# Kernel tuning notes

Hardware: AMD Instinct MI355X
Metric: run time of the kernel (lower is better)

## Reference

```python
import jax, jax.numpy as jnp
import numpy as np

DIM = 2048
N_HEADS = 16
N_KV_HEADS = 4
HEAD_DIM = DIM // N_HEADS  # 128
ROPE_BASE = 10000.0
QK_GAIN_INIT = 1.0
RMS_EPS = 1.1920928955078125e-07  # torch F.rms_norm default eps = finfo(fp32).eps


def _rms_norm(x):
    # normalize over last dim, no learned gain
    var = jnp.mean(jnp.square(x), axis=-1, keepdims=True)
    return x * jax.lax.rsqrt(var + RMS_EPS)


def _rope_cos_sin(seq_len, dtype):
    half = HEAD_DIM // 2
    inv_freq = 1.0 / (ROPE_BASE ** (jnp.arange(0, HEAD_DIM, 2, dtype=jnp.float32) / HEAD_DIM))
    t = jnp.arange(seq_len, dtype=jnp.float32)
    freqs = jnp.outer(t, inv_freq)  # [S, half]
    return jnp.cos(freqs).astype(dtype), jnp.sin(freqs).astype(dtype)


def _apply_rotary(x, cos, sin):
    # x: [B, H, S, D]; cos/sin: [S, D//2] broadcast over B,H
    half = x.shape[-1] // 2
    x1, x2 = x[..., :half], x[..., half:]
    return jnp.concatenate((x1 * cos + x2 * sin, x1 * (-sin) + x2 * cos), axis=-1)


def setup_inputs() -> dict:
    key = jax.random.key(0)
    ks = jax.random.split(key, 6)
    B, S = 2, 2048
    kv_dim = N_KV_HEADS * HEAD_DIM
    x = jax.random.normal(ks[0], (B, S, DIM), dtype=jnp.float32)
    Wq = jax.random.normal(ks[1], (DIM, DIM), dtype=jnp.float32) * (DIM ** -0.5)
    Wk = jax.random.normal(ks[2], (kv_dim, DIM), dtype=jnp.float32) * (DIM ** -0.5)
    Wv = jax.random.normal(ks[3], (kv_dim, DIM), dtype=jnp.float32) * (DIM ** -0.5)
    Wproj = jax.random.normal(ks[4], (DIM, DIM), dtype=jnp.float32) * (DIM ** -0.5)
    q_gain = jnp.full((N_HEADS,), QK_GAIN_INIT, dtype=jnp.float32)
    return {"x": x, "Wq": Wq, "Wk": Wk, "Wv": Wv, "Wproj": Wproj, "q_gain": q_gain}


def reference(x, Wq, Wk, Wv, Wproj, q_gain):
    B, S, D = x.shape
    G = N_HEADS // N_KV_HEADS  # GQA group size
    # QKV projections (CastedLinear, no bias)
    q = (x @ Wq.T).reshape(B, S, N_HEADS, HEAD_DIM).transpose(0, 2, 1, 3)      # [B,H,S,d]
    k = (x @ Wk.T).reshape(B, S, N_KV_HEADS, HEAD_DIM).transpose(0, 2, 1, 3)   # [B,Hkv,S,d]
    v = (x @ Wv.T).reshape(B, S, N_KV_HEADS, HEAD_DIM).transpose(0, 2, 1, 3)
    # QK RMS-norm
    q = _rms_norm(q)
    k = _rms_norm(k)
    # RoPE (scaling='none' -> attention_factor = 1.0)
    cos, sin = _rope_cos_sin(S, q.dtype)
    q = _apply_rotary(q, cos, sin)
    k = _apply_rotary(k, cos, sin)
    # per-head query gain * attention_factor (=1.0)
    q = q * q_gain.astype(q.dtype)[None, :, None, None]
    # causal GQA SDPA: group queries by kv head, no k/v materialized repeats
    qg = q.reshape(B, N_KV_HEADS, G, S, HEAD_DIM)
    scale = 1.0 / jnp.sqrt(jnp.asarray(HEAD_DIM, dtype=q.dtype))
    scores = jnp.einsum('bkgqd,bkld->bkgql', qg, k) * scale  # [B,Hkv,G,S,S]
    causal = jnp.tril(jnp.ones((S, S), dtype=bool))
    scores = jnp.where(causal, scores, jnp.asarray(-jnp.inf, dtype=scores.dtype))
    attn = jax.nn.softmax(scores, axis=-1)
    y = jnp.einsum('bkgql,bkld->bkgqd', attn, v)              # [B,Hkv,G,S,d]
    y = y.reshape(B, N_HEADS, S, HEAD_DIM).transpose(0, 2, 1, 3).reshape(B, S, D)
    return y @ Wproj.T
```

## Files before the change

### kernel.cpp

```cpp
#include <hip/hip_runtime.h>
#include <hip/hip_bf16.h>

#define DIM 2048
#define NH 16
#define NKV 4
#define HD 128
#define S_LEN 2048
#define BATCH 2
#define QKV_N 3072
#define NEGBIG -1.0e30f

typedef __attribute__((ext_vector_type(8))) short bf16x8;
typedef __attribute__((ext_vector_type(4))) float f32x4;
typedef unsigned short ushort_t;

#define GLOAD_LDS16(gp, lp)                                                       \
    __builtin_amdgcn_global_load_lds(                                             \
        (const __attribute__((address_space(1))) void*)(gp),                      \
        (__attribute__((address_space(3))) void*)(lp), 16, 0, 0)

static __device__ __forceinline__ ushort_t f2bf(float f) {
    union { float f; unsigned u; } v; v.f = f;
    unsigned r = v.u + 0x7fffu + ((v.u >> 16) & 1u);
    return (ushort_t)(r >> 16);
}
static __device__ __forceinline__ float bf2f(ushort_t u) {
    union { unsigned u; float f; } v; v.u = ((unsigned)u) << 16;
    return v.f;
}
static __device__ __forceinline__ unsigned pk2bf(float a, float b) {
    unsigned r;
    __asm__ volatile("v_cvt_pk_bf16_f32 %0, %1, %2" : "=v"(r) : "v"(a), "v"(b));
    return r;
}

__global__ __launch_bounds__(256) void cvt_in(const float* __restrict__ x,
                                              const float* __restrict__ Wq,
                                              const float* __restrict__ Wk,
                                              const float* __restrict__ Wv,
                                              const float* __restrict__ Wp,
                                              ushort_t* __restrict__ xb,
                                              ushort_t* __restrict__ Wqkvb,
                                              ushort_t* __restrict__ Wpb) {
    int i = (blockIdx.x * 256 + threadIdx.x) * 4;
    const float* src;
    ushort_t* dst;
    int soff, doff;
    if (i < 8388608) {
        src = x; dst = xb; soff = i; doff = i;
    } else if (i < 14680064) {
        int j = i - 8388608;
        dst = Wqkvb; doff = j;
        if (j < 4194304) { src = Wq; soff = j; }
        else if (j < 5242880) { src = Wk; soff = j - 4194304; }
        else { src = Wv; soff = j - 5242880; }
    } else {
        int j = i - 14680064;
        src = Wp; dst = Wpb; soff = j; doff = j;
    }
    float4 v = *(const float4*)&src[soff];
    uint2 o = {pk2bf(v.x, v.y), pk2bf(v.z, v.w)};
    *(uint2*)&dst[doff] = o;
}

static __device__ __forceinline__ void store_c(float* p, float v) { *p = v; }
static __device__ __forceinline__ void store_c(ushort_t* p, float v) { *p = f2bf(v); }

template <typename OutT>
__global__ __launch_bounds__(256) void gemm_bt(const ushort_t* __restrict__ A,
                                               const ushort_t* __restrict__ B,
                                               OutT* __restrict__ C,
                                               int M, int N, int K) {
    __shared__ __align__(16) ushort_t As[128 * 64];
    __shared__ __align__(16) ushort_t Bs[128 * 64];
    const int t = threadIdx.x;
    const int lane = t & 63;
    const int wave = t >> 6;
    const int m16 = lane & 15;
    const int quad = lane >> 4;
    const int wr = wave >> 1;
    const int wc = wave & 1;
    const int m0 = blockIdx.y * 128;
    const int n0 = blockIdx.x * 128;

    f32x4 acc[4][4];
#pragma unroll
    for (int i = 0; i < 4; i++)
#pragma unroll
        for (int j = 0; j < 4; j++) acc[i][j] = (f32x4){0.f, 0.f, 0.f, 0.f};

    const int rsub = lane >> 3;
    const int csw0 = lane & 7;

    for (int k0 = 0; k0 < K; k0 += 64) {
#pragma unroll
        for (int i = 0; i < 4; ++i) {
            const int rowb = wave * 32 + i * 8;
            const int row = rowb + rsub;
            const int gc = (csw0 ^ (row & 7)) * 8;
            GLOAD_LDS16(&A[(size_t)(m0 + row) * K + k0 + gc], &As[rowb * 64]);
            GLOAD_LDS16(&B[(size_t)(n0 + row) * K + k0 + gc], &Bs[rowb * 64]);
        }
        __syncthreads();
#pragma unroll
        for (int ks = 0; ks < 2; ks++) {
            bf16x8 af[4], bfr[4];
#pragma unroll
            for (int mt = 0; mt < 4; mt++) {
                const int row = wr * 64 + mt * 16 + m16;
                af[mt] = *(const bf16x8*)&As[row * 64 + (((ks * 4 + quad) ^ (row & 7)) * 8)];
            }
#pragma unroll
            for (int nt = 0; nt < 4; nt++) {
                const int row = wc * 64 + nt * 16 + m16;
                bfr[nt] = *(const bf16x8*)&Bs[row * 64 + (((ks * 4 + quad) ^ (row & 7)) * 8)];
            }
#pragma unroll
            for (int mt = 0; mt < 4; mt++)
#pragma unroll
                for (int nt = 0; nt < 4; nt++)
                    acc[mt][nt] = __builtin_amdgcn_mfma_f32_16x16x32_bf16(af[mt], bfr[nt],
                                                                          acc[mt][nt], 0, 0, 0);
        }
        __syncthreads();
    }
#pragma unroll
    for (int mt = 0; mt < 4; mt++) {
#pragma unroll
        for (int r = 0; r < 4; r++) {
            int row = m0 + wr * 64 + mt * 16 + quad * 4 + r;
#pragma unroll
            for (int nt = 0; nt < 4; nt++) {
                int col = n0 + wc * 64 + nt * 16 + m16;
                store_c(&C[(size_t)row * N + col], acc[mt][nt][r]);
            }
        }
    }
}

__global__ __launch_bounds__(256) void gemm_qkv(const ushort_t* __restrict__ A,
                                                const ushort_t* __restrict__ B,
                                                ushort_t* __restrict__ qkv,
                                                ushort_t* __restrict__ vt,
                                                const float* __restrict__ gain) {
    __shared__ __align__(16) ushort_t sh[2][128 * 64];
    ushort_t* As = sh[0];
    ushort_t* Bs = sh[1];
    ushort_t* Cs = &sh[0][0];
    const int t = threadIdx.x;
    const int lane = t & 63;
    const int wave = t >> 6;
    const int m16 = lane & 15;
    const int quad = lane >> 4;
    const int wr = wave >> 1;
    const int wc = wave & 1;
    const int m0 = blockIdx.y * 128;
    const int bx = blockIdx.x;
    const int n0 = bx * 128;
    const int K = DIM;

    f32x4 acc[4][4];
#pragma unroll
    for (int i = 0; i < 4; i++)
#pragma unroll
        for (int j = 0; j < 4; j++) acc[i][j] = (f32x4){0.f, 0.f, 0.f, 0.f};

    const int rsub = lane >> 3;
    const int csw0 = lane & 7;

    for (int k0 = 0; k0 < K; k0 += 64) {
#pragma unroll
        for (int i = 0; i < 4; ++i) {
            const int rowb = wave * 32 + i * 8;
            const int row = rowb + rsub;
            const int gc = (csw0 ^ (row & 7)) * 8;
            GLOAD_LDS16(&A[(size_t)(m0 + row) * K + k0 + gc], &As[rowb * 64]);
            GLOAD_LDS16(&B[(size_t)(n0 + row) * K + k0 + gc], &Bs[rowb * 64]);
        }
        __syncthreads();
#pragma unroll
        for (int ks = 0; ks < 2; ks++) {
            bf16x8 af[4], bfr[4];
#pragma unroll
            for (int mt = 0; mt < 4; mt++) {
                const int row = wr * 64 + mt * 16 + m16;
                af[mt] = *(const bf16x8*)&As[row * 64 + (((ks * 4 + quad) ^ (row & 7)) * 8)];
            }
#pragma unroll
            for (int nt = 0; nt < 4; nt++) {
                const int row = wc * 64 + nt * 16 + m16;
                bfr[nt] = *(const bf16x8*)&Bs[row * 64 + (((ks * 4 + quad) ^ (row & 7)) * 8)];
            }
#pragma unroll
            for (int mt = 0; mt < 4; mt++)
#pragma unroll
                for (int nt = 0; nt < 4; nt++)
                    acc[mt][nt] = __builtin_amdgcn_mfma_f32_16x16x32_bf16(af[mt], bfr[nt],
                                                                          acc[mt][nt], 0, 0, 0);
        }
        __syncthreads();
    }
#pragma unroll
    for (int mt = 0; mt < 4; mt++)
#pragma unroll
        for (int r = 0; r < 4; r++) {
            const int row = wr * 64 + mt * 16 + quad * 4 + r;
#pragma unroll
            for (int nt = 0; nt < 4; nt++)
                Cs[row * 128 + wc * 64 + nt * 16 + m16] = f2bf(acc[mt][nt][r]);
        }
    __syncthreads();

    if (bx < 20) {
        const float g = (bx < 16) ? gain[bx] : 1.0f;
        const float invf = exp2f(-0.20762050593046f * (float)lane);
#pragma unroll 4
        for (int i = 0; i < 32; i++) {
            const int row = wave * 32 + i;
            const int m = m0 + row;
            const int s = m & (S_LEN - 1);
            float x1 = bf2f(Cs[row * 128 + lane]);
            float x2 = bf2f(Cs[row * 128 + lane + 64]);
            float ss = x1 * x1 + x2 * x2;
#pragma unroll
            for (int mm = 32; mm >= 1; mm >>= 1) ss += __shfl_xor(ss, mm, 64);
            const float rms = rsqrtf(ss * (1.0f / 128.0f) + 1.1920928955078125e-07f);
            x1 *= rms; x2 *= rms;
            const float fr = (float)s * invf;
            const float c = cosf(fr), sn = sinf(fr);
            ushort_t* dst = qkv + (size_t)m * QKV_N + bx * 128;
            dst[lane] = f2bf((x1 * c + x2 * sn) * g);
            dst[lane + 64] = f2bf((x2 * c - x1 * sn) * g);
        }
    } else {
        const int d = t >> 1;
        const int so = (t & 1) * 64;
        const int b = m0 >> 11;
        const int s0 = m0 & (S_LEN - 1);
        const int kv = bx - 20;
        ushort_t* dst = vt + ((size_t)(b * NKV + kv) * HD + d) * S_LEN + s0 + so;
#pragma unroll
        for (int j0 = 0; j0 < 64; j0 += 8) {
            ushort_t tmp[8];
#pragma unroll
            for (int j = 0; j < 8; j++) tmp[j] = Cs[(so + j0 + j) * 128 + d];
            *(uint4*)&dst[j0] = *(uint4*)tmp;
        }
    }
}

__device__ __constant__ short attn_tab[24][4] = {
    {15, 0, 16, 14}, {15, 16, 32, 15}, {7, 0, 16, -1}, {14, 0, 15, 12},
    {13, 0, 14, 10}, {13, 14, 28, 11}, {6, 0, 14, -1}, {10, 0, 11, 4},
    {12, 0, 13, 8},  {12, 13, 26, 9}, {14, 15, 30, 13}, {11, 0, 12, 6},
    {11, 12, 24, 7}, {5, 0, 12, -1}, {10, 11, 22, 5},  {9, 0, 10, 2},
    {2, 0, 6, -1},   {1, 0, 4, -1},  {0, 0, 2, -1},    {3, 0, 8, -1},
    {8, 0, 9, 0},    {8, 9, 18, 1},  {9, 10, 20, 3},   {4, 0, 10, -1},
};

__global__ __launch_bounds__(256) void attn(const ushort_t* __restrict__ QKV,
                                            const ushort_t* __restrict__ Vt,
                                            ushort_t* __restrict__ Y,
                                            ushort_t* __restrict__ Po,
                                            float* __restrict__ Pl) {
    __shared__ __align__(16) ushort_t Ks[64 * 128];
    __shared__ __align__(16) ushort_t Vs[128 * 64];
    __shared__ __align__(16) ushort_t Ps[4][32 * 72];
    const int lane = threadIdx.x & 63;
    const int wave = threadIdx.x >> 6;
    const int m16 = lane & 15, quad = lane >> 4;
    const int seg = blockIdx.x >> 5;
    const int hb = blockIdx.x & 31;
    const int h = hb & (NH - 1), b = hb >> 4;
    const int kvh = h >> 2;
    const int bx = attn_tab[seg][0];
    const int t0 = attn_tab[seg][1];
    const int t1 = attn_tab[seg][2];
    const int slotl = attn_tab[seg][3];
    const int q0w = bx * 128 + wave * 32;

    const ushort_t* kbase = QKV + (size_t)b * S_LEN * QKV_N + DIM + kvh * HD;
    const ushort_t* vbase = Vt + (size_t)(b * NKV + kvh) * (HD * S_LEN);

    bf16x8 bq[2][4];
#pragma unroll
    for (int g = 0; g < 2; g++)
#pragma unroll
        for (int ks = 0; ks < 4; ks++)
            bq[g][ks] = *(const bf16x8*)&QKV[((size_t)(b * S_LEN + q0w + g * 16 + m16)) * QKV_N +
                                             h * HD + ks * 32 + quad * 8];

    float ls[2] = {0.f, 0.f};
    f32x4 o[2][8];
#pragma unroll
    for (int g = 0; g < 2; g++)
#pragma unroll
        for (int nd = 0; nd < 8; nd++) o[g][nd] = (f32x4){0.f, 0.f, 0.f, 0.f};

    ushort_t* pw = Ps[wave];
    for (int t = t0; t < t1; ++t) {
        const int kv0 = t * 64;
        __syncthreads();
#pragma unroll
        for (int i = 0; i < 4; i++) {
            const int c0 = i * 256 + wave * 64;
            const int ck = c0 + lane;
            const int krow = ck >> 4;
            const int kcol = (ck & 15) ^ (krow & 7);
            GLOAD_LDS16(kbase + (size_t)(kv0 + krow) * QKV_N + kcol * 8, &Ks[c0 * 8]);
            const int vd = ck >> 3;
            const int vcol = (ck & 7) ^ (vd & 7);
            GLOAD_LDS16(vbase + (size_t)vd * S_LEN + kv0 + vcol * 8, &Vs[c0 * 8]);
        }
        __syncthreads();

        f32x4 st[2][4];
#pragma unroll
        for (int g = 0; g < 2; g++)
#pragma unroll
            for (int nt = 0; nt < 4; nt++) st[g][nt] = (f32x4){0.f, 0.f, 0.f, 0.f};
#pragma unroll
        for (int ks = 0; ks < 4; ks++)
#pragma unroll
            for (int nt = 0; nt < 4; nt++) {
                const int row = nt * 16 + m16;
                bf16x8 ak = *(const bf16x8*)&Ks[row * 128 + (((ks * 4 + quad) ^ (row & 7)) * 8)];
#pragma unroll
                for (int g = 0; g < 2; g++)
                    st[g][nt] = __builtin_amdgcn_mfma_f32_16x16x32_bf16(ak, bq[g][ks],
                                                                        st[g][nt], 0, 0, 0);
            }
#pragma unroll
        for (int g = 0; g < 2; g++) {
            const int q0g = q0w + g * 16;
            const int qg = q0g + m16;
            const bool interior = (kv0 + 63 <= q0g);
            float rs = 0.f;
#pragma unroll
            for (int nt = 0; nt < 4; nt++) {
                float p[4];
#pragma unroll
                for (int r = 0; r < 4; r++) {
                    float x = st[g][nt][r] * 0.08838834764831845f;
                    if (!interior) {
                        const int kg = kv0 + nt * 16 + quad * 4 + r;
                        x = (kg > qg) ? NEGBIG : x;
                    }
                    p[r] = __expf(x);
                }
                rs += (p[0] + p[1]) + (p[2] + p[3]);
                uint2 pk = {pk2bf(p[0], p[1]), pk2bf(p[2], p[3])};
                *(uint2*)&pw[(g * 16 + m16) * 72 + nt * 16 + quad * 4] = pk;
            }
            ls[g] += rs;
        }
        __asm__ __volatile__("s_waitcnt lgkmcnt(0)" ::: "memory");
        bf16x8 bp[2][2];
#pragma unroll
        for (int g = 0; g < 2; g++)
#pragma unroll
            for (int kk = 0; kk < 2; kk++)
                bp[g][kk] = *(const bf16x8*)&pw[(g * 16 + m16) * 72 + kk * 32 + quad * 8];
#pragma unroll
        for (int kk = 0; kk < 2; kk++)
#pragma unroll
            for (int nd = 0; nd < 8; nd++) {
                const int vrow = nd * 16 + m16;
                bf16x8 av = *(const bf16x8*)&Vs[vrow * 64 + (((kk * 4 + quad) ^ (vrow & 7)) * 8)];
#pragma unroll
                for (int g = 0; g < 2; g++)
                    o[g][nd] = __builtin_amdgcn_mfma_f32_16x16x32_bf16(av, bp[g][kk],
                                                                       o[g][nd], 0, 0, 0);
            }
    }
    float l_tot[2];
#pragma unroll
    for (int g = 0; g < 2; g++) {
        float v = ls[g];
        v += __shfl_xor(v, 16, 64);
        v += __shfl_xor(v, 32, 64);
        l_tot[g] = v;
    }
    if (slotl < 0) {
#pragma unroll
        for (int g = 0; g < 2; g++) {
            const float inv = 1.0f / l_tot[g];
            const int qg = q0w + g * 16 + m16;
            ushort_t* yp = Y + ((size_t)(b * S_LEN + qg)) * DIM + h * HD;
#pragma unroll
            for (int nd = 0; nd < 8; nd++) {
                uint2 pk = {pk2bf(o[g][nd][0] * inv, o[g][nd][1] * inv),
                            pk2bf(o[g][nd][2] * inv, o[g][nd][3] * inv)};
                *(uint2*)&yp[nd * 16 + quad * 4] = pk;
            }
        }
    } else if ((slotl & 1) == 0) {
        const int slot = ((b * NH + h) << 4) + slotl;
#pragma unroll
        for (int g = 0; g < 2; g++) {
            const int qg = q0w + g * 16 + m16;
            ushort_t* yp = Y + ((size_t)(b * S_LEN + qg)) * DIM + h * HD;
#pragma unroll
            for (int nd = 0; nd < 8; nd++) {
                uint2 pk = {pk2bf(o[g][nd][0], o[g][nd][1]),
                            pk2bf(o[g][nd][2], o[g][nd][3])};
                *(uint2*)&yp[nd * 16 + quad * 4] = pk;
            }
            if (quad == 0) Pl[slot * 128 + wave * 32 + g * 16 + m16] = l_tot[g];
        }
    } else {
        const int slot = ((b * NH + h) << 4) + slotl;
        ushort_t* po = Po + (size_t)(((b * NH + h) << 3) + (slotl >> 1)) * (128 * 128);
#pragma unroll
        for (int g = 0; g < 2; g++) {
            const int ql = wave * 32 + g * 16 + m16;
#pragma unroll
            for (int nd = 0; nd < 8; nd++) {
                uint2 pk = {pk2bf(o[g][nd][0], o[g][nd][1]),
                            pk2bf(o[g][nd][2], o[g][nd][3])};
                *(uint2*)&po[ql * 128 + nd * 16 + quad * 4] = pk;
            }
            if (quad == 0) Pl[slot * 128 + ql] = l_tot[g];
        }
    }
}

__global__ __launch_bounds__(256) void attn_combine(const ushort_t* __restrict__ Po,
                                                    const float* __restrict__ Pl,
                                                    ushort_t* __restrict__ Y) {
    const int R = blockIdx.x * 2 + (threadIdx.x >> 7);
    const int d = threadIdx.x & 127;
    const int q = R & 127;
    const int bx8 = (R >> 7) & 7;
    const int h = (R >> 10) & 15;
    const int b = R >> 14;
    const int hb16 = ((b * NH + h) << 4);
    const float l0 = Pl[(hb16 + bx8 * 2) * 128 + q];
    const float l1 = Pl[(hb16 + bx8 * 2 + 1) * 128 + q];
    const float inv = 1.0f / (l0 + l1);
    const int qg = (bx8 + 8) * 128 + q;
    ushort_t* yp = Y + ((size_t)(b * S_LEN + qg)) * DIM + h * HD + d;
    const float o0 = bf2f(*yp);
    const float o1 = bf2f(Po[(size_t)(((b * NH + h) << 3) + bx8) * (128 * 128) + q * 128 + d]);
    *yp = f2bf((o0 + o1) * inv);
}

extern "C" void kernel_launch(void* const* d_in, const int* in_sizes, int n_in,
                              void* d_out, int out_size, void* d_ws, size_t ws_size,
                              hipStream_t stream) {
    (void)in_sizes; (void)n_in; (void)out_size; (void)ws_size;
    const float* xf  = (const float*)d_in[0];
    const float* Wqf = (const float*)d_in[1];
    const float* Wkf = (const float*)d_in[2];
    const float* Wvf = (const float*)d_in[3];
    const float* Wpf = (const float*)d_in[4];
    const float* gn  = (const float*)d_in[5];
    float* out = (float*)d_out;

    char* ws = (char*)d_ws;
    ushort_t* xb    = (ushort_t*)(ws);
    ushort_t* qkv   = (ushort_t*)(ws + (16ull << 20));
    ushort_t* vt    = (ushort_t*)(ws + (40ull << 20));
    ushort_t* Wqkvb = (ushort_t*)(ws + (44ull << 20));
    ushort_t* Wpb   = (ushort_t*)(ws + (56ull << 20));
    ushort_t* y     = xb;
    ushort_t* Po    = (ushort_t*)(ws + (44ull << 20));
    float*    Pl    = (float*)(ws + (52ull << 20));

    const int M = BATCH * S_LEN;
    cvt_in<<<dim3(18432), 256, 0, stream>>>(xf, Wqf, Wkf, Wvf, Wpf, xb, Wqkvb, Wpb);
    gemm_qkv<<<dim3(QKV_N / 128, M / 128), 256, 0, stream>>>(xb, Wqkvb, qkv, vt, gn);
    attn<<<dim3(768, 1, 1), 256, 0, stream>>>(qkv, vt, y, Po, Pl);
    attn_combine<<<dim3(BATCH * NH * 8 * 128 / 2), 256, 0, stream>>>(Po, Pl, y);
    gemm_bt<<<dim3(DIM / 128, M / 128), 256, 0, stream>>>(y, Wpb, out, M, DIM, DIM);
}
```

Measured before the change: 309.7 us.

## Replace both GEMMs with a 256x256-tile double-buffered pipelined MFMA kernel

Both the QKV projection and the output projection now use one templated GEMM with 256x256 tiles, 512 threads and two LDS buffers. Global-to-LDS loads for the next K step are issued in quarter-tile pieces, interleaved with MFMA sub-steps, using explicit vmcnt waits, barriers and setprio. The aim is to hide memory latency behind compute and to reuse more data per tile. The cost is higher register and LDS pressure and fewer blocks: 192 for QKV and 128 for the output projection, which may underfill the CU count.

```diff
diff --git a/kernel.cpp b/kernel.cpp
--- a/kernel.cpp
+++ b/kernel.cpp
@@ -63,188 +63,218 @@
     *(uint2*)&dst[doff] = o;
 }
 
-static __device__ __forceinline__ void store_c(float* p, float v) { *p = v; }
-static __device__ __forceinline__ void store_c(ushort_t* p, float v) { *p = f2bf(v); }
-
-template <typename OutT>
-__global__ __launch_bounds__(256) void gemm_bt(const ushort_t* __restrict__ A,
-                                               const ushort_t* __restrict__ B,
-                                               OutT* __restrict__ C,
-                                               int M, int N, int K) {
-    __shared__ __align__(16) ushort_t As[128 * 64];
-    __shared__ __align__(16) ushort_t Bs[128 * 64];
+#define FENCE() __asm__ __volatile__("" ::: "memory")
+#define BARRIER() do { FENCE(); __builtin_amdgcn_s_barrier(); FENCE(); } while (0)
+#define WAITVM(n) __asm__ __volatile__("s_waitcnt vmcnt(" #n ")" ::: "memory")
+#define WLGKM0() __asm__ __volatile__("s_waitcnt lgkmcnt(0)" ::: "memory")
+
+#define STG(LDSA, GP, rowb) do {                                                  \
+    const int r_ = (rowb) + rsub;                                                 \
+    GLOAD_LDS16(&(GP)[(size_t)r_ * 2048 + kk0_ + ((csw0 ^ (r_ & 7)) * 8)],        \
+                &(LDSA)[(rowb) * 64]);                                            \
+} while (0)
+
+#define STAGE_HT(AB, BB, kt, ht) do {                                             \
+    const int kt_ = (kt) < 31 ? (kt) : 31;                                        \
+    const int kk0_ = kt_ * 64;                                                    \
+    if ((ht) == 0)      { STG(BB, Bp, w8);       STG(BB, Bp, 64 + w8);  }         \
+    else if ((ht) == 1) { STG(BB, Bp, 128 + w8); STG(BB, Bp, 192 + w8); }         \
+    else if ((ht) == 2) { STG(AB, Ap, w8);       STG(AB, Ap, 128 + w8); }         \
+    else                { STG(AB, Ap, 64 + w8);  STG(AB, Ap, 192 + w8); }         \
+} while (0)
+
+#define DSA(mtb, AS) do {                                                         \
+    _Pragma("unroll") for (int dm = 0; dm < 2; dm++)                              \
+    _Pragma("unroll") for (int ks = 0; ks < 2; ks++) {                            \
+        const int row = wr * 128 + ((mtb) + dm) * 16 + m16;                       \
+        af[dm][ks] = *(const bf16x8*)&(AS)[row * 64 +                             \
+                                           (((ks * 4 + quad) ^ (row & 7)) * 8)];  \
+    }                                                                             \
+} while (0)
+
+#define DSB(BS) do {                                                              \
+    _Pragma("unroll") for (int nt = 0; nt < 4; nt++)                              \
+    _Pragma("unroll") for (int ks = 0; ks < 2; ks++) {                            \
+        const int row = wc * 64 + nt * 16 + m16;                                  \
+        bfr[nt][ks] = *(const bf16x8*)&(BS)[row * 64 +                            \
+                                            (((ks * 4 + quad) ^ (row & 7)) * 8)]; \
+    }                                                                             \
+} while (0)
+
+#define MMA(mtb) do {                                                             \
+    __builtin_amdgcn_s_setprio(1);                                                \
+    _Pragma("unroll") for (int ks = 0; ks < 2; ks++)                              \
+    _Pragma("unroll") for (int dm = 0; dm < 2; dm++)                              \
+    _Pragma("unroll") for (int nt = 0; nt < 4; nt++)                              \
+        acc[(mtb) + dm][nt] = __builtin_amdgcn_mfma_f32_16x16x32_bf16(            \
+            af[dm][ks], bfr[nt][ks], acc[(mtb) + dm][nt], 0, 0, 0);               \
+    __builtin_amdgcn_s_setprio(0);                                                \
+} while (0)
+
+template <int EPI>
+__global__ __launch_bounds__(512, 2) void gemm256(const ushort_t* __restrict__ A,
+                                                  const ushort_t* __restrict__ B,
+                                                  float* __restrict__ C,
+                                                  ushort_t* __restrict__ qkv,
+                                                  ushort_t* __restrict__ vt,
+                                                  const float* __restrict__ gain,
+                                                  int N) {
+    __shared__ __align__(16) ushort_t sh[4][256 * 64];
     const int t = threadIdx.x;
     const int lane = t & 63;
     const int wave = t >> 6;
     const int m16 = lane & 15;
     const int quad = lane >> 4;
-    const int wr = wave >> 1;
-    const int wc = wave & 1;
-    const int m0 = blockIdx.y * 128;
-    const int n0 = blockIdx.x * 128;
-
-    f32x4 acc[4][4];
-#pragma unroll
-    for (int i = 0; i < 4; i++)
-#pragma unroll
-        for (int j = 0; j < 4; j++) acc[i][j] = (f32x4){0.f, 0.f, 0.f, 0.f};
-
+    const int wr = wave >> 2;
+    const int wc = wave & 3;
+    const int m0 = blockIdx.y * 256;
+    const int bx = blockIdx.x;
+    const int n0 = bx * 256;
     const int rsub = lane >> 3;
     const int csw0 = lane & 7;
-
-    for (int k0 = 0; k0 < K; k0 += 64) {
-#pragma unroll
-        for (int i = 0; i < 4; ++i) {
-            const int rowb = wave * 32 + i * 8;
-            const int row = rowb + rsub;
-            const int gc = (csw0 ^ (row & 7)) * 8;
-            GLOAD_LDS16(&A[(size_t)(m0 + row) * K + k0 + gc], &As[rowb * 64]);
-            GLOAD_LDS16(&B[(size_t)(n0 + row) * K + k0 + gc], &Bs[rowb * 64]);
-        }
+    const int w8 = wave * 8;
+    const ushort_t* Ap = A + (size_t)m0 * 2048;
+    const ushort_t* Bp = B + (size_t)n0 * 2048;
+
+    f32x4 acc[8][4];
+#pragma unroll
+    for (int i = 0; i < 8; i++)
+#pragma unroll
+        for (int j = 0; j < 4; j++) acc[i][j] = (f32x4){0.f, 0.f, 0.f, 0.f};
+
+    STAGE_HT(sh[0], sh[2], 0, 0);
+    STAGE_HT(sh[0], sh[2], 0, 1);
+    STAGE_HT(sh[0], sh[2], 0, 2);
+    STAGE_HT(sh[0], sh[2], 0, 3);
+    STAGE_HT(sh[1], sh[3], 1, 0);
+    STAGE_HT(sh[1], sh[3], 1, 1);
+    STAGE_HT(sh[1], sh[3], 1, 2);
+    WAITVM(6);
+    BARRIER();
+
+    bf16x8 bfr[4][2];
+#pragma unroll 1
+    for (int i = 0; i < 16; ++i) {
+        const int tb = 2 * i;
+        {
+            bf16x8 af[2][2];
+            DSA(0, sh[0]); DSB(sh[2]);
+            STAGE_HT(sh[1], sh[3], tb + 1, 3);
+            BARRIER(); WLGKM0(); MMA(0); BARRIER();
+        }
+        {
+            bf16x8 af[2][2];
+            DSA(2, sh[0]);
+            STAGE_HT(sh[0], sh[2], tb + 2, 0);
+            BARRIER(); WLGKM0(); MMA(2); BARRIER();
+        }
+        {
+            bf16x8 af[2][2];
+            DSA(4, sh[0]);
+            STAGE_HT(sh[0], sh[2], tb + 2, 1);
+            BARRIER(); WLGKM0(); MMA(4); BARRIER();
+        }
+        {
+            bf16x8 af[2][2];
+            DSA(6, sh[0]);
+            STAGE_HT(sh[0], sh[2], tb + 2, 2);
+            WAITVM(6);
+            BARRIER(); WLGKM0(); MMA(6); BARRIER();
+        }
+        {
+            bf16x8 af[2][2];
+            DSA(0, sh[1]); DSB(sh[3]);
+            STAGE_HT(sh[0], sh[2], tb + 2, 3);
+            BARRIER(); WLGKM0(); MMA(0); BARRIER();
+        }
+        {
+            bf16x8 af[2][2];
+            DSA(2, sh[1]);
+            STAGE_HT(sh[1], sh[3], tb + 3, 0);
+            BARRIER(); WLGKM0(); MMA(2); BARRIER();
+        }
+        {
+            bf16x8 af[2][2];
+            DSA(4, sh[1]);
+            STAGE_HT(sh[1], sh[3], tb + 3, 1);
+            BARRIER(); WLGKM0(); MMA(4); BARRIER();
+        }
+        {
+            bf16x8 af[2][2];
+            DSA(6, sh[1]);
+            STAGE_HT(sh[1], sh[3], tb + 3, 2);
+            WAITVM(6);
+            BARRIER(); WLGKM0(); MMA(6); BARRIER();
+        }
+    }
+    WAITVM(0);
+    __syncthreads();
+
+    if constexpr (EPI == 0) {
+#pragma unroll
+        for (int mt = 0; mt < 8; mt++)
+#pragma unroll
+            for (int r = 0; r < 4; r++) {
+                const int row = m0 + wr * 128 + mt * 16 + quad * 4 + r;
+#pragma unroll
+                for (int nt = 0; nt < 4; nt++)
+                    C[(size_t)row * N + n0 + wc * 64 + nt * 16 + m16] = acc[mt][nt][r];
+            }
+    } else {
+        ushort_t* Cs = &sh[0][0];
+#pragma unroll
+        for (int mt = 0; mt < 8; mt++)
+#pragma unroll
+            for (int r = 0; r < 4; r++) {
+                const int row = wr * 128 + mt * 16 + quad * 4 + r;
+#pragma unroll
+                for (int nt = 0; nt < 4; nt++)
+                    Cs[row * 256 + wc * 64 + nt * 16 + m16] = f2bf(acc[mt][nt][r]);
+            }
         __syncthreads();
-#pragma unroll
-        for (int ks = 0; ks < 2; ks++) {
-            bf16x8 af[4], bfr[4];
-#pragma unroll
-            for (int mt = 0; mt < 4; mt++) {
-                const int row = wr * 64 + mt * 16 + m16;
-                af[mt] = *(const bf16x8*)&As[row * 64 + (((ks * 4 + quad) ^ (row & 7)) * 8)];
-            }
-#pragma unroll
-            for (int nt = 0; nt < 4; nt++) {
-                const int row = wc * 64 + nt * 16 + m16;
-                bfr[nt] = *(const bf16x8*)&Bs[row * 64 + (((ks * 4 + quad) ^ (row & 7)) * 8)];
-            }
-#pragma unroll
-            for (int mt = 0; mt < 4; mt++)
-#pragma unroll
-                for (int nt = 0; nt < 4; nt++)
-                    acc[mt][nt] = __builtin_amdgcn_mfma_f32_16x16x32_bf16(af[mt], bfr[nt],
-                                                                          acc[mt][nt], 0, 0, 0);
-        }
-        __syncthreads();
-    }
-#pragma unroll
-    for (int mt = 0; mt < 4; mt++) {
-#pragma unroll
-        for (int r = 0; r < 4; r++) {
-            int row = m0 + wr * 64 + mt * 16 + quad * 4 + r;
-#pragma unroll
-            for (int nt = 0; nt < 4; nt++) {
-                int col = n0 + wc * 64 + nt * 16 + m16;
-                store_c(&C[(size_t)row * N + col], acc[mt][nt][r]);
-            }
-        }
-    }
-}
-
-__global__ __launch_bounds__(256) void gemm_qkv(const ushort_t* __restrict__ A,
-                                                const ushort_t* __restrict__ B,
-                                                ushort_t* __restrict__ qkv,
-                                                ushort_t* __restrict__ vt,
-                                                const float* __restrict__ gain) {
-    __shared__ __align__(16) ushort_t sh[2][128 * 64];
-    ushort_t* As = sh[0];
-    ushort_t* Bs = sh[1];
-    ushort_t* Cs = &sh[0][0];
-    const int t = threadIdx.x;
-    const int lane = t & 63;
-    const int wave = t >> 6;
-    const int m16 = lane & 15;
-    const int quad = lane >> 4;
-    const int wr = wave >> 1;
-    const int wc = wave & 1;
-    const int m0 = blockIdx.y * 128;
-    const int bx = blockIdx.x;
-    const int n0 = bx * 128;
-    const int K = DIM;
-
-    f32x4 acc[4][4];
-#pragma unroll
-    for (int i = 0; i < 4; i++)
-#pragma unroll
-        for (int j = 0; j < 4; j++) acc[i][j] = (f32x4){0.f, 0.f, 0.f, 0.f};
-
-    const int rsub = lane >> 3;
-    const int csw0 = lane & 7;
-
-    for (int k0 = 0; k0 < K; k0 += 64) {
-#pragma unroll
-        for (int i = 0; i < 4; ++i) {
-            const int rowb = wave * 32 + i * 8;
-            const int row = rowb + rsub;
-            const int gc = (csw0 ^ (row & 7)) * 8;
-            GLOAD_LDS16(&A[(size_t)(m0 + row) * K + k0 + gc], &As[rowb * 64]);
-            GLOAD_LDS16(&B[(size_t)(n0 + row) * K + k0 + gc], &Bs[rowb * 64]);
-        }
-        __syncthreads();
-#pragma unroll
-        for (int ks = 0; ks < 2; ks++) {
-            bf16x8 af[4], bfr[4];
-#pragma unroll
-            for (int mt = 0; mt < 4; mt++) {
-                const int row = wr * 64 + mt * 16 + m16;
-                af[mt] = *(const bf16x8*)&As[row * 64 + (((ks * 4 + quad) ^ (row & 7)) * 8)];
-            }
-#pragma unroll
-            for (int nt = 0; nt < 4; nt++) {
-                const int row = wc * 64 + nt * 16 + m16;
-                bfr[nt] = *(const bf16x8*)&Bs[row * 64 + (((ks * 4 + quad) ^ (row & 7)) * 8)];
-            }
-#pragma unroll
-            for (int mt = 0; mt < 4; mt++)
-#pragma unroll
-                for (int nt = 0; nt < 4; nt++)
-                    acc[mt][nt] = __builtin_amdgcn_mfma_f32_16x16x32_bf16(af[mt], bfr[nt],
-                                                                          acc[mt][nt], 0, 0, 0);
-        }
-        __syncthreads();
-    }
-#pragma unroll
-    for (int mt = 0; mt < 4; mt++)
-#pragma unroll
-        for (int r = 0; r < 4; r++) {
-            const int row = wr * 64 + mt * 16 + quad * 4 + r;
-#pragma unroll
-            for (int nt = 0; nt < 4; nt++)
-                Cs[row * 128 + wc * 64 + nt * 16 + m16] = f2bf(acc[mt][nt][r]);
-        }
-    __syncthreads();
-
-    if (bx < 20) {
-        const float g = (bx < 16) ? gain[bx] : 1.0f;
-        const float invf = exp2f(-0.20762050593046f * (float)lane);
-#pragma unroll 4
-        for (int i = 0; i < 32; i++) {
-            const int row = wave * 32 + i;
-            const int m = m0 + row;
-            const int s = m & (S_LEN - 1);
-            float x1 = bf2f(Cs[row * 128 + lane]);
-            float x2 = bf2f(Cs[row * 128 + lane + 64]);
-            float ss = x1 * x1 + x2 * x2;
-#pragma unroll
-            for (int mm = 32; mm >= 1; mm >>= 1) ss += __shfl_xor(ss, mm, 64);
-            const float rms = rsqrtf(ss * (1.0f / 128.0f) + 1.1920928955078125e-07f);
-            x1 *= rms; x2 *= rms;
-            const float fr = (float)s * invf;
-            const float c = cosf(fr), sn = sinf(fr);
-            ushort_t* dst = qkv + (size_t)m * QKV_N + bx * 128;
-            dst[lane] = f2bf((x1 * c + x2 * sn) * g);
-            dst[lane + 64] = f2bf((x2 * c - x1 * sn) * g);
-        }
-    } else {
-        const int d = t >> 1;
-        const int so = (t & 1) * 64;
-        const int b = m0 >> 11;
-        const int s0 = m0 & (S_LEN - 1);
-        const int kv = bx - 20;
-        ushort_t* dst = vt + ((size_t)(b * NKV + kv) * HD + d) * S_LEN + s0 + so;
-#pragma unroll
-        for (int j0 = 0; j0 < 64; j0 += 8) {
-            ushort_t tmp[8];
-#pragma unroll
-            for (int j = 0; j < 8; j++) tmp[j] = Cs[(so + j0 + j) * 128 + d];
-            *(uint4*)&dst[j0] = *(uint4*)tmp;
+
+        if (bx < 10) {
+            const float invf = exp2f(-0.20762050593046f * (float)lane);
+            float gg[2];
+#pragma unroll
+            for (int hh = 0; hh < 2; hh++) gg[hh] = (bx < 8) ? gain[bx * 2 + hh] : 1.0f;
+#pragma unroll 2
+            for (int i = 0; i < 32; i++) {
+                const int row = wave * 32 + i;
+                const int m = m0 + row;
+                const int s = m & (S_LEN - 1);
+                const float fr = (float)s * invf;
+                const float c = cosf(fr), sn = sinf(fr);
+#pragma unroll
+                for (int hh = 0; hh < 2; hh++) {
+                    float x1 = bf2f(Cs[row * 256 + hh * 128 + lane]);
+                    float x2 = bf2f(Cs[row * 256 + hh * 128 + 64 + lane]);
+                    float ss = x1 * x1 + x2 * x2;
+#pragma unroll
+                    for (int mm = 32; mm >= 1; mm >>= 1) ss += __shfl_xor(ss, mm, 64);
+                    const float rms = rsqrtf(ss * (1.0f / 128.0f) + 1.1920928955078125e-07f);
+                    x1 *= rms; x2 *= rms;
+                    ushort_t* dst = qkv + (size_t)m * QKV_N + bx * 256 + hh * 128;
+                    dst[lane] = f2bf((x1 * c + x2 * sn) * gg[hh]);
+                    dst[lane + 64] = f2bf((x2 * c - x1 * sn) * gg[hh]);
+                }
+            }
+        } else {
+            const int half = t >> 8;
+            const int tt = t & 255;
+            const int d = tt >> 1;
+            const int so = (tt & 1) * 128;
+            const int b = m0 >> 11;
+            const int s0 = m0 & (S_LEN - 1);
+            const int kv = (bx - 10) * 2 + half;
+            ushort_t* dst = vt + ((size_t)(b * NKV + kv) * HD + d) * S_LEN + s0 + so;
+#pragma unroll
+            for (int j0 = 0; j0 < 128; j0 += 8) {
+                ushort_t tmp[8];
+#pragma unroll
+                for (int j = 0; j < 8; j++) tmp[j] = Cs[(so + j0 + j) * 256 + half * 128 + d];
+                *(uint4*)&dst[j0] = *(uint4*)tmp;
+            }
         }
     }
 }
@@ -469,8 +499,8 @@
 
     const int M = BATCH * S_LEN;
     cvt_in<<<dim3(18432), 256, 0, stream>>>(xf, Wqf, Wkf, Wvf, Wpf, xb, Wqkvb, Wpb);
-    gemm_qkv<<<dim3(QKV_N / 128, M / 128), 256, 0, stream>>>(xb, Wqkvb, qkv, vt, gn);
+    gemm256<1><<<dim3(QKV_N / 256, M / 256), 512, 0, stream>>>(xb, Wqkvb, nullptr, qkv, vt, gn, 0);
     attn<<<dim3(768, 1, 1), 256, 0, stream>>>(qkv, vt, y, Po, Pl);
     attn_combine<<<dim3(BATCH * NH * 8 * 128 / 2), 256, 0, stream>>>(Po, Pl, y);
-    gemm_bt<<<dim3(DIM / 128, M / 128), 256, 0, stream>>>(y, Wpb, out, M, DIM, DIM);
-}
+    gemm256<0><<<dim3(DIM / 256, M / 256), 512, 0, stream>>>(y, Wpb, out, nullptr, nullptr, nullptr, DIM);
+}
```

New measurement: 308.2 us. No clear change (-0.5%).
